# Performance work log

Measured on AMD Instinct MI355X. Metric: run time of the kernel, lower is better.

## Reference

```python
import jax, jax.numpy as jnp
import numpy as np

B, L, D, Y = 8, 2500, 512, 8921


def setup_inputs() -> dict:
    key = jax.random.key(0)
    k1, k2, k3, k4, k5 = jax.random.split(key, 5)
    x = jax.random.normal(k1, (B, L, D), dtype=jnp.float32)
    target = jax.random.uniform(k2, (B, Y), dtype=jnp.float32)
    U_w = jax.random.normal(k3, (Y, D), dtype=jnp.float32) * (1.0 / np.sqrt(D))
    final_w = jax.random.normal(k4, (Y, D), dtype=jnp.float32) * (1.0 / np.sqrt(D))
    final_b = jax.random.normal(k5, (Y,), dtype=jnp.float32) * 0.01
    return {"x": x, "target": target, "text_inputs": 0,
            "U_w": U_w, "final_w": final_w, "final_b": final_b}


def _bce_with_logits(y, t):
    # stable mean BCE-with-logits, matching torch BCEWithLogitsLoss (reduction='mean')
    return jnp.mean(jnp.maximum(y, 0.0) - y * t + jnp.log1p(jnp.exp(-jnp.abs(y))))


def reference(x, target, text_inputs, U_w, final_w, final_b):
    # label-wise attention scores: [B, Y, L]
    scores = jnp.einsum('yd,bld->byl', U_w, x)
    alpha = jax.nn.softmax(scores, axis=-1)
    # attended context per label: [B, Y, D]
    m = jnp.einsum('byl,bld->byd', alpha, x)
    # per-label dot-product readout: [B, Y]
    y = jnp.einsum('yd,byd->by', final_w, m) + final_b
    loss = _bce_with_logits(y, target)
    return (y, loss)
```

## Files before the change

### kernel.cpp

```cpp
#include <hip/hip_runtime.h>
#include <math.h>

#define B_  8
#define L_  2500
#define D_  512
#define Y_  8921
#define LP  2560
#define YP  8960

#define WS_F16_HALVES  (B_ * LP * D_ + 2 * YP * D_)
#define ACC_FLOATS     (2 * B_ * YP)

typedef _Float16 f16x8 __attribute__((ext_vector_type(8)));
typedef float    f32x4 __attribute__((ext_vector_type(4)));

__device__ __forceinline__ void load_lds16(const _Float16* g, _Float16* l) {
  __builtin_amdgcn_global_load_lds(
      (const __attribute__((address_space(1))) unsigned int*)g,
      (__attribute__((address_space(3))) unsigned int*)l, 16, 0, 0);
}

__global__ void k_convert(const float* __restrict__ x,
                          const float* __restrict__ Uw,
                          const float* __restrict__ Fw,
                          _Float16* __restrict__ ws,
                          float* __restrict__ loss_slot) {
  if (blockIdx.x == 0 && threadIdx.x == 0) *loss_slot = 0.0f;
  const int NX = B_ * LP * (D_ / 8);
  int idx = blockIdx.x * 256 + threadIdx.x;
  if (idx < ACC_FLOATS) ((float*)(ws + WS_F16_HALVES))[idx] = 0.0f;
  const float* src = nullptr;
  if (idx < NX) {
    int b  = idx / (LP * 64);
    int r  = idx - b * (LP * 64);
    int l  = r >> 6;
    int d8 = r & 63;
    if (l < L_) src = x + (((long)b * L_ + l) * D_ + d8 * 8);
  } else {
    int u    = idx - NX;
    int lane = u & 63;
    int mi   = (u >> 6) & 7;
    int kk2  = (u >> 9) & 15;
    int yt   = u >> 13;
    int grow = yt * 128 + mi * 16 + (lane & 15);
    int sub  = grow & 15;
    int y    = (grow >> 4) * 8 + (sub & 7);
    int k8   = kk2 * 4 + (lane >> 4);
    if (y < Y_) src = (sub < 8 ? Uw : Fw) + (long)y * D_ + k8 * 8;
  }
  f16x8 o;
  if (src) {
    const float4* s4 = (const float4*)src;
    float4 a = s4[0], c = s4[1];
    o[0] = (_Float16)a.x; o[1] = (_Float16)a.y; o[2] = (_Float16)a.z; o[3] = (_Float16)a.w;
    o[4] = (_Float16)c.x; o[5] = (_Float16)c.y; o[6] = (_Float16)c.z; o[7] = (_Float16)c.w;
  } else {
    for (int i = 0; i < 8; ++i) o[i] = (_Float16)0.0f;
  }
  ((f16x8*)ws)[idx] = o;
}

__global__ __launch_bounds__(256, 2)
void k_attn(const _Float16* __restrict__ ws,
            float* __restrict__ accG) {
  __shared__ __align__(16) _Float16 XT[16384];

  const int tid  = threadIdx.x;
  const int lane = tid & 63;
  const int wave = tid >> 6;
  const int wy = wave & 1;
  const int wl = wave >> 1;
  const int yt = blockIdx.x;
  const int b  = blockIdx.y;
  const int lh = blockIdx.z;

  const _Float16* Xg = ws + (long)b * LP * D_ + (long)lh * (LP / 2) * D_;
  const _Float16* Ga = ws + (long)B_ * LP * D_ + (long)yt * (128 * 512)
                          + (wy * 4) * 512 + lane * 8;

  const int srow = lane >> 3;
  const int sg8  = ((lane & 7) ^ srow) * 8;
  const _Float16* xsrc[8];
  _Float16*       xdst[8];
  #pragma unroll
  for (int i = 0; i < 8; ++i) {
    int seg = wave * 8 + i;
    xsrc[i] = Xg + (long)(seg * 8 + srow) * D_ + sg8;
    xdst[i] = XT + seg * 512;
  }

  const int xrow = wl * 128 + (lane & 15);
  const int r7   = lane & 7;
  const int gb   = lane >> 4;
  const bool sLow = (lane < 32);

  float redP[4][4];
  #pragma unroll
  for (int i = 0; i < 4; ++i)
    for (int v = 0; v < 4; ++v) redP[i][v] = 0.0f;

  for (int lt = 0; lt < 5; ++lt) {
    f32x4 acc[4][8];
    #pragma unroll
    for (int mi = 0; mi < 4; ++mi)
      for (int ni = 0; ni < 8; ++ni) {
        f32x4 z = {0.0f, 0.0f, 0.0f, 0.0f};
        acc[mi][ni] = z;
      }
    const long xofs = (long)lt * 256 * D_;
    for (int kkstep = 0; kkstep < 8; ++kkstep) {
      f16x8 au[2][4];
      #pragma unroll
      for (int ks = 0; ks < 2; ++ks)
        #pragma unroll
        for (int mi = 0; mi < 4; ++mi)
          au[ks][mi] = *(const f16x8*)(Ga + (size_t)(kkstep * 2 + ks) * 4096 + mi * 512);
      __syncthreads();
      #pragma unroll
      for (int i = 0; i < 8; ++i)
        load_lds16(xsrc[i] + xofs + kkstep * 64, xdst[i]);
      __syncthreads();
      #pragma unroll
      for (int ks = 0; ks < 2; ++ks) {
        int off = (((ks * 4 + gb) ^ r7) * 8);
        f16x8 bx[8];
        #pragma unroll
        for (int ni = 0; ni < 8; ++ni)
          bx[ni] = *(const f16x8*)&XT[(xrow + ni * 16) * 64 + off];
        #pragma unroll
        for (int mi = 0; mi < 4; ++mi)
          #pragma unroll
          for (int ni = 0; ni < 8; ++ni)
            acc[mi][ni] = __builtin_amdgcn_mfma_f32_16x16x32_f16(au[ks][mi], bx[ni], acc[mi][ni], 0, 0, 0);
      }
    }
    #pragma unroll
    for (int mi = 0; mi < 4; ++mi)
      for (int ni = 0; ni < 8; ++ni)
        #pragma unroll
        for (int v = 0; v < 4; ++v) {
          float a = acc[mi][ni][v];
          float e = __expf(a);
          float p = __shfl_xor(e, 32, 64);
          redP[mi][v] += sLow ? e : p * a;
        }
  }

  for (int m = 1; m < 16; m <<= 1)
    #pragma unroll
    for (int mi = 0; mi < 4; ++mi)
      for (int v = 0; v < 4; ++v)
        redP[mi][v] += __shfl_xor(redP[mi][v], m, 64);
  if ((lane & 15) == 0) {
    float* dst = accG + (sLow ? 0 : B_ * YP);
    #pragma unroll
    for (int mi = 0; mi < 4; ++mi)
      for (int v = 0; v < 4; ++v) {
        int y = yt * 64 + wy * 32 + mi * 8 + ((lane >> 4) & 1) * 4 + v;
        atomicAdd(&dst[b * YP + y], redP[mi][v]);
      }
  }
}

__global__ void k_final(const float* __restrict__ accG,
                        const float* __restrict__ fb,
                        float* __restrict__ out) {
  int id = blockIdx.x * 256 + threadIdx.x;
  if (id >= B_ * Y_) return;
  int b = id / Y_, y = id - b * Y_;
  float den = accG[b * YP + y] - (float)(LP - L_);
  out[id] = accG[B_ * YP + b * YP + y] / den + fb[y];
}

__global__ void k_loss(const float* __restrict__ y,
                       const float* __restrict__ t,
                       float* __restrict__ loss) {
  float p = 0.0f;
  for (int i = blockIdx.x * 256 + threadIdx.x; i < B_ * Y_; i += gridDim.x * 256) {
    float v = y[i], tg = t[i];
    p += fmaxf(v, 0.0f) - v * tg + log1pf(__expf(-fabsf(v)));
  }
  for (int m = 32; m; m >>= 1) p += __shfl_down(p, m, 64);
  __shared__ float wsum[4];
  int lane = threadIdx.x & 63, wv = threadIdx.x >> 6;
  if (lane == 0) wsum[wv] = p;
  __syncthreads();
  if (threadIdx.x == 0) {
    float s = wsum[0] + wsum[1] + wsum[2] + wsum[3];
    atomicAdd(loss, s * (1.0f / (float)(B_ * Y_)));
  }
}

extern "C" void kernel_launch(void* const* d_in, const int* in_sizes, int n_in,
                              void* d_out, int out_size, void* d_ws, size_t ws_size,
                              hipStream_t stream) {
  (void)in_sizes; (void)n_in; (void)out_size; (void)ws_size;
  const float* x       = (const float*)d_in[0];
  const float* target  = (const float*)d_in[1];
  const float* U_w     = (const float*)d_in[3];
  const float* final_w = (const float*)d_in[4];
  const float* final_b = (const float*)d_in[5];
  float* out = (float*)d_out;
  _Float16* ws = (_Float16*)d_ws;
  float* accG = (float*)(ws + WS_F16_HALVES);

  k_convert<<<9600, 256, 0, stream>>>(x, U_w, final_w, ws, out + B_ * Y_);

  dim3 g(YP / 64, B_, 2);
  k_attn<<<g, 256, 0, stream>>>(ws, accG);

  k_final<<<(B_ * Y_ + 255) / 256, 256, 0, stream>>>(accG, final_b, out);
  k_loss<<<140, 256, 0, stream>>>(out, target, out + B_ * Y_);
}
```

Measured before the change: 546.3 us.

## Double-buffer X tiles in LDS with async prefetch of next K step

Doubles the LDS tile buffer so the next X slice is loaded with global_load_lds while the current slice feeds MFMAs. Partial vmcnt waits and raw s_barrier replace the two __syncthreads per step, and s_setprio raises wave priority around the MFMA block. LDS use doubles to 64KB per block, which may limit occupancy at two blocks per CU. The reliance on vmcnt counting with the interleaved U loads is fragile.

```diff
diff --git a/kernel.cpp b/kernel.cpp
--- a/kernel.cpp
+++ b/kernel.cpp
@@ -63,7 +63,7 @@
 __global__ __launch_bounds__(256, 2)
 void k_attn(const _Float16* __restrict__ ws,
             float* __restrict__ accG) {
-  __shared__ __align__(16) _Float16 XT[16384];
+  __shared__ __align__(16) _Float16 XT[2][16384];
 
   const int tid  = threadIdx.x;
   const int lane = tid & 63;
@@ -80,14 +80,8 @@
 
   const int srow = lane >> 3;
   const int sg8  = ((lane & 7) ^ srow) * 8;
-  const _Float16* xsrc[8];
-  _Float16*       xdst[8];
-  #pragma unroll
-  for (int i = 0; i < 8; ++i) {
-    int seg = wave * 8 + i;
-    xsrc[i] = Xg + (long)(seg * 8 + srow) * D_ + sg8;
-    xdst[i] = XT + seg * 512;
-  }
+  const _Float16* xbase = Xg + (long)(wave * 64 + srow) * D_ + sg8;
+  _Float16* lbase = &XT[0][wave * 4096];
 
   const int xrow = wl * 128 + (lane & 15);
   const int r7   = lane & 7;
@@ -98,6 +92,10 @@
   #pragma unroll
   for (int i = 0; i < 4; ++i)
     for (int v = 0; v < 4; ++v) redP[i][v] = 0.0f;
+
+  #pragma unroll
+  for (int i = 0; i < 8; ++i)
+    load_lds16(xbase + i * 4096, lbase + i * 512);
 
   for (int lt = 0; lt < 5; ++lt) {
     f32x4 acc[4][8];
@@ -107,43 +105,57 @@
         f32x4 z = {0.0f, 0.0f, 0.0f, 0.0f};
         acc[mi][ni] = z;
       }
-    const long xofs = (long)lt * 256 * D_;
-    for (int kkstep = 0; kkstep < 8; ++kkstep) {
+    #pragma unroll 2
+    for (int kk = 0; kk < 8; ++kk) {
+      const int s   = lt * 8 + kk;
+      const int cur = kk & 1;
       f16x8 au[2][4];
       #pragma unroll
       for (int ks = 0; ks < 2; ++ks)
         #pragma unroll
         for (int mi = 0; mi < 4; ++mi)
-          au[ks][mi] = *(const f16x8*)(Ga + (size_t)(kkstep * 2 + ks) * 4096 + mi * 512);
-      __syncthreads();
-      #pragma unroll
-      for (int i = 0; i < 8; ++i)
-        load_lds16(xsrc[i] + xofs + kkstep * 64, xdst[i]);
-      __syncthreads();
+          au[ks][mi] = *(const f16x8*)(Ga + (size_t)(kk * 2 + ks) * 4096 + mi * 512);
+      __builtin_amdgcn_sched_barrier(0);
+      {
+        const int  sp  = (s < 39) ? s + 1 : 39;
+        const long ofs = (long)(sp >> 3) * (256 * D_) + (long)(sp & 7) * 64;
+        _Float16* dst = lbase + (cur ^ 1) * 16384;
+        #pragma unroll
+        for (int i = 0; i < 8; ++i)
+          load_lds16(xbase + ofs + i * 4096, dst + i * 512);
+      }
+      asm volatile("s_waitcnt vmcnt(8)" ::: "memory");
+      __builtin_amdgcn_s_barrier();
+      __builtin_amdgcn_sched_barrier(0);
+      __builtin_amdgcn_s_setprio(1);
       #pragma unroll
       for (int ks = 0; ks < 2; ++ks) {
-        int off = (((ks * 4 + gb) ^ r7) * 8);
+        const int off = (((ks * 4 + gb) ^ r7) * 8);
         f16x8 bx[8];
         #pragma unroll
         for (int ni = 0; ni < 8; ++ni)
-          bx[ni] = *(const f16x8*)&XT[(xrow + ni * 16) * 64 + off];
+          bx[ni] = *(const f16x8*)&XT[cur][(xrow + ni * 16) * 64 + off];
         #pragma unroll
         for (int mi = 0; mi < 4; ++mi)
           #pragma unroll
           for (int ni = 0; ni < 8; ++ni)
             acc[mi][ni] = __builtin_amdgcn_mfma_f32_16x16x32_f16(au[ks][mi], bx[ni], acc[mi][ni], 0, 0, 0);
       }
+      __builtin_amdgcn_s_setprio(0);
+      if (kk == 7) {
+        #pragma unroll
+        for (int mi = 0; mi < 4; ++mi)
+          for (int ni = 0; ni < 8; ++ni)
+            #pragma unroll
+            for (int v = 0; v < 4; ++v) {
+              float a = acc[mi][ni][v];
+              float e = __expf(a);
+              float p = __shfl_xor(e, 32, 64);
+              redP[mi][v] += sLow ? e : p * a;
+            }
+      }
+      __builtin_amdgcn_s_barrier();
     }
-    #pragma unroll
-    for (int mi = 0; mi < 4; ++mi)
-      for (int ni = 0; ni < 8; ++ni)
-        #pragma unroll
-        for (int v = 0; v < 4; ++v) {
-          float a = acc[mi][ni][v];
-          float e = __expf(a);
-          float p = __shfl_xor(e, 32, 64);
-          redP[mi][v] += sLow ? e : p * a;
-        }
   }
 
   for (int m = 1; m < 16; m <<= 1)
```

Result: no change. 555.3 us (+1.6%).
